# Kernel optimization log

Measured on AMD Instinct MI355X. Metric: run time of the kernel, lower is better.

Reference implementation:

```python
import jax, jax.numpy as jnp
import numpy as np

N = 6144          # nodes
F_IN = 512        # num_feature
HID = 64          # hidden_dim
C = 40            # num_class
H = 3             # num_heads
ALPHA = 0.2       # leaky relu slope
NEG_INF = -9e15


def gat_layer(x, adj, W, a_src, a_dst):
    # x: [N, f_in], W: [H, f_in, f_out], a_src/a_dst: [H, f_out]
    Wh = jnp.einsum('nf,hfo->hno', x, W)                  # [H, N, f_out]
    e_src = jnp.einsum('hno,ho->hn', Wh, a_src)           # [H, N]
    e_dst = jnp.einsum('hno,ho->hn', Wh, a_dst)           # [H, N]
    e = jax.nn.leaky_relu(e_src[:, :, None] + e_dst[:, None, :], ALPHA)  # [H, N, N]
    scores = jnp.where(adj > 0, e, NEG_INF)               # mask non-edges
    attn = jax.nn.softmax(scores, axis=-1)                # softmax over neighbors
    out = jnp.einsum('hnm,hmo->hno', attn, Wh)            # [H, N, f_out]
    return out.mean(axis=0)                               # average heads -> [N, f_out]


def setup_inputs() -> dict:
    key = jax.random.key(0)
    k = jax.random.split(key, 8)
    feature = jax.random.normal(k[0], (N, F_IN), dtype=jnp.float32)
    adj = (jax.random.uniform(k[1], (N, N)) < 0.01).astype(jnp.float32)
    adj = jnp.maximum(adj, jnp.eye(N, dtype=jnp.float32))
    s1 = 1.0 / np.sqrt(F_IN)
    s2 = 1.0 / np.sqrt(HID)
    W1 = jax.random.normal(k[2], (H, F_IN, HID), dtype=jnp.float32) * s1
    a1_src = jax.random.normal(k[3], (H, HID), dtype=jnp.float32) * s2
    a1_dst = jax.random.normal(k[4], (H, HID), dtype=jnp.float32) * s2
    W2 = jax.random.normal(k[5], (H, HID, C), dtype=jnp.float32) * s2
    a2_src = jax.random.normal(k[6], (H, C), dtype=jnp.float32) * (1.0 / np.sqrt(C))
    a2_dst = jax.random.normal(k[7], (H, C), dtype=jnp.float32) * (1.0 / np.sqrt(C))
    return {"feature": feature, "adj": adj, "W1": W1, "a1_src": a1_src,
            "a1_dst": a1_dst, "W2": W2, "a2_src": a2_src, "a2_dst": a2_dst}


def reference(feature, adj, W1, a1_src, a1_dst, W2, a2_src, a2_dst):
    # eval mode: dropout is identity
    x = jax.nn.relu(gat_layer(feature, adj, W1, a1_src, a1_dst))  # [N, HID]
    x = gat_layer(x, adj, W2, a2_src, a2_dst)                     # [N, C]
    return jax.nn.log_softmax(x, axis=1)
```

## Files before the change

### kernel.cpp

```cpp
#include <hip/hip_runtime.h>
#include <math.h>

#define NN   6144
#define FIN  512
#define HIDN 64
#define NC   40
#define NH   3
#define CAP  128
#define NCHUNK (CAP / 64)
#define LALPHA 0.2f
#define KSPLIT 4
#define PK_LOW  0x3FFFu
#define PK_HIGH 0xFFFFC000u

typedef unsigned long long ull;

__device__ __forceinline__ float bf2f(ushort s) {
    return __uint_as_float((unsigned)s << 16);
}
__device__ __forceinline__ ushort f2bf(float f) {
    unsigned u = __float_as_uint(f);
    return (ushort)((u + 0x7FFFu + ((u >> 16) & 1u)) >> 16);
}

__global__ __launch_bounds__(256) void k_csr(const float* __restrict__ adj,
                                             int* __restrict__ nbr,
                                             int* __restrict__ deg) {
    __shared__ int lidx[4][64];
    __shared__ int wtot[4];
    int row  = blockIdx.x;
    int wid  = threadIdx.x >> 6;
    int lane = threadIdx.x & 63;
    const float* base = adj + (size_t)row * NN + wid * (NN / 4);
    ull below = (1ull << lane) - 1ull;
    int cnt = 0;
#pragma unroll
    for (int ch = 0; ch < 6; ch++) {
        float4 v = *reinterpret_cast<const float4*>(base + ch * 256 + lane * 4);
        bool h0 = v.x > 0.f, h1 = v.y > 0.f, h2 = v.z > 0.f, h3 = v.w > 0.f;
        ull b0 = __ballot(h0), b1 = __ballot(h1), b2 = __ballot(h2), b3 = __ballot(h3);
        int p = cnt + __popcll(b0 & below) + __popcll(b1 & below)
                    + __popcll(b2 & below) + __popcll(b3 & below);
        int col = wid * (NN / 4) + ch * 256 + lane * 4;
        if (h0) { if (p < 64) lidx[wid][p] = col + 0; p++; }
        if (h1) { if (p < 64) lidx[wid][p] = col + 1; p++; }
        if (h2) { if (p < 64) lidx[wid][p] = col + 2; p++; }
        if (h3) { if (p < 64) lidx[wid][p] = col + 3; p++; }
        cnt += __popcll(b0) + __popcll(b1) + __popcll(b2) + __popcll(b3);
    }
    if (lane == 0) wtot[wid] = cnt;
    __syncthreads();
    int t0 = wtot[0], t1 = wtot[1], t2 = wtot[2], t3 = wtot[3];
    int wb = (wid > 0 ? t0 : 0) + (wid > 1 ? t1 : 0) + (wid > 2 ? t2 : 0);
    int total = t0 + t1 + t2 + t3;
    if (threadIdx.x == 0) deg[row] = total < CAP ? total : CAP;
    int myc = wtot[wid] < 64 ? wtot[wid] : 64;
    if (lane < myc) {
        int pos = wb + lane;
        if (pos < CAP) nbr[(size_t)row * CAP + pos] = lidx[wid][lane];
    }
}

__global__ __launch_bounds__(256) void k_gemm1(const float* __restrict__ x,
                                               const float* __restrict__ W,
                                               float* __restrict__ Whp) {
    __shared__ float xs[64][68];
    __shared__ float wsh[64][68];
    int h  = blockIdx.y;
    int n0 = blockIdx.x * 64;
    int kz = blockIdx.z;
    int tid = threadIdx.x;
    int og4 = (tid & 15) * 4;
    int mg4 = (tid >> 4) * 4;

    float acc[4][4] = {{0.f}};
    const float* xbase0 = x + (size_t)n0 * FIN;
    const float* wbase0 = W + (size_t)h * FIN * HIDN;

    for (int t = 0; t < 2; t++) {
        int k0 = kz * 128 + t * 64;
#pragma unroll
        for (int i = 0; i < 4; i++) {
            int l = tid + i * 256;
            int r = l >> 4;
            int c = (l & 15) * 4;
            *reinterpret_cast<float4*>(&xs[r][c]) =
                *reinterpret_cast<const float4*>(xbase0 + (size_t)r * FIN + k0 + c);
            *reinterpret_cast<float4*>(&wsh[r][c]) =
                *reinterpret_cast<const float4*>(wbase0 + (size_t)(k0 + r) * HIDN + c);
        }
        __syncthreads();

#pragma unroll 8
        for (int k = 0; k < 64; k += 4) {
            float4 xv[4], wv[4];
            xv[0] = *reinterpret_cast<const float4*>(&xs[mg4 + 0][k]);
            xv[1] = *reinterpret_cast<const float4*>(&xs[mg4 + 1][k]);
            xv[2] = *reinterpret_cast<const float4*>(&xs[mg4 + 2][k]);
            xv[3] = *reinterpret_cast<const float4*>(&xs[mg4 + 3][k]);
            wv[0] = *reinterpret_cast<const float4*>(&wsh[k + 0][og4]);
            wv[1] = *reinterpret_cast<const float4*>(&wsh[k + 1][og4]);
            wv[2] = *reinterpret_cast<const float4*>(&wsh[k + 2][og4]);
            wv[3] = *reinterpret_cast<const float4*>(&wsh[k + 3][og4]);
            const float* xf = reinterpret_cast<const float*>(xv);
            const float* wf = reinterpret_cast<const float*>(wv);
#pragma unroll
            for (int i = 0; i < 4; i++) {
#pragma unroll
                for (int kk = 0; kk < 4; kk++) {
                    float xval = xf[i * 4 + kk];
#pragma unroll
                    for (int j = 0; j < 4; j++)
                        acc[i][j] += xval * wf[kk * 4 + j];
                }
            }
        }
        __syncthreads();
    }

    float* outp = Whp + (((size_t)kz * NH + h) * NN + n0 + mg4) * HIDN + og4;
#pragma unroll
    for (int i = 0; i < 4; i++) {
        float4 v = make_float4(acc[i][0], acc[i][1], acc[i][2], acc[i][3]);
        *reinterpret_cast<float4*>(outp + (size_t)i * HIDN) = v;
    }
}

__global__ __launch_bounds__(256) void k_sum_e1(const float* __restrict__ Whp,
                                                const float* __restrict__ a_src,
                                                const float* __restrict__ a_dst,
                                                ushort* __restrict__ Whb,
                                                float* __restrict__ es,
                                                float* __restrict__ ed) {
    int gw   = blockIdx.x * 4 + (threadIdx.x >> 6);
    int lane = threadIdx.x & 63;
    int h = gw / NN, n = gw % NN;
    size_t idx = ((size_t)h * NN + n) * HIDN + lane;
    size_t stride = (size_t)NH * NN * HIDN;
    float v = Whp[idx] + Whp[idx + stride] + Whp[idx + 2 * stride] + Whp[idx + 3 * stride];
    Whb[idx] = f2bf(v);
    float s = v * a_src[h * HIDN + lane];
    float d = v * a_dst[h * HIDN + lane];
#pragma unroll
    for (int off = 32; off; off >>= 1) {
        s += __shfl_xor(s, off);
        d += __shfl_xor(d, off);
    }
    if (lane == 0) { es[h * NN + n] = s; ed[h * NN + n] = d; }
}

__global__ __launch_bounds__(192) void k_attn1f(const int* __restrict__ nbr,
                                                const int* __restrict__ deg,
                                                const ushort* __restrict__ Whb,
                                                const float* __restrict__ es,
                                                const float* __restrict__ ed,
                                                const float* __restrict__ W2,
                                                const float* __restrict__ a2s,
                                                const float* __restrict__ a2d,
                                                ushort* __restrict__ Wh2b,
                                                float* __restrict__ e2s,
                                                float* __restrict__ e2d) {
    __shared__ unsigned pks[NH][CAP];
    __shared__ float hsum[NH][HIDN];
    int n = blockIdx.x;
    int h = threadIdx.x >> 6;
    int lane = threadIdx.x & 63;
    int d = deg[n];
    const int* nrow = nbr + (size_t)n * CAP;
    float esv = es[h * NN + n];

    float psum = 0.f;
#pragma unroll
    for (int c = 0; c < NCHUNK; c++) {
        int k = c * 64 + lane;
        unsigned u = 0;
        if (k < d) {
            int mm = nrow[k];
            float e = esv + ed[h * NN + mm];
            float s = e > 0.f ? e : LALPHA * e;
            float p = __expf(s);
            u = (__float_as_uint(p) & PK_HIGH) | (unsigned)mm;
            psum += __uint_as_float(u & PK_HIGH);
        }
        pks[h][k] = u;
    }
#pragma unroll
    for (int off = 32; off; off >>= 1) psum += __shfl_xor(psum, off);
    float inv = 1.f / psum;
    __syncthreads();

    const ushort* WhH = Whb + (size_t)h * NN * HIDN + lane;
    float a0 = 0.f, a1 = 0.f, a2 = 0.f, a3 = 0.f;
    int iters = (d + 3) >> 2;
    for (int g = 0; g < iters; g++) {
        uint4 uu = *reinterpret_cast<const uint4*>(&pks[h][g * 4]);
        a0 += __uint_as_float(uu.x & PK_HIGH) * bf2f(WhH[(size_t)(uu.x & PK_LOW) * HIDN]);
        a1 += __uint_as_float(uu.y & PK_HIGH) * bf2f(WhH[(size_t)(uu.y & PK_LOW) * HIDN]);
        a2 += __uint_as_float(uu.z & PK_HIGH) * bf2f(WhH[(size_t)(uu.z & PK_LOW) * HIDN]);
        a3 += __uint_as_float(uu.w & PK_HIGH) * bf2f(WhH[(size_t)(uu.w & PK_LOW) * HIDN]);
    }
    float hacc = ((a0 + a1) + (a2 + a3));
    hsum[h][lane] = hacc * inv;
    __syncthreads();

    float xv = (hsum[0][lane] + hsum[1][lane] + hsum[2][lane]) * (1.f / NH);
    xv = fmaxf(xv, 0.f);

    int c = lane < NC ? lane : NC - 1;
    float acc = 0.f;
#pragma unroll 8
    for (int o = 0; o < HIDN; o++) {
        float xb = __shfl(xv, o);
        float wv = W2[((size_t)h * HIDN + o) * NC + c];
        acc += xb * wv;
    }
    if (lane >= NC) acc = 0.f;

    float s2 = acc * (lane < NC ? a2s[h * NC + lane] : 0.f);
    float d2 = acc * (lane < NC ? a2d[h * NC + lane] : 0.f);
#pragma unroll
    for (int off = 32; off; off >>= 1) {
        s2 += __shfl_xor(s2, off);
        d2 += __shfl_xor(d2, off);
    }
    if (lane < NC) Wh2b[((size_t)h * NN + n) * NC + lane] = f2bf(acc);
    if (lane == 0) { e2s[h * NN + n] = s2; e2d[h * NN + n] = d2; }
}

__global__ __launch_bounds__(192) void k_attn2(const int* __restrict__ nbr,
                                               const int* __restrict__ deg,
                                               const ushort* __restrict__ Wh2b,
                                               const float* __restrict__ es,
                                               const float* __restrict__ ed,
                                               float* __restrict__ out) {
    __shared__ unsigned pks[NH][CAP];
    __shared__ float hsum[NH][HIDN];
    int n = blockIdx.x;
    int h = threadIdx.x >> 6;
    int lane = threadIdx.x & 63;
    int d = deg[n];
    const int* nrow = nbr + (size_t)n * CAP;
    float esv = es[h * NN + n];

    float psum = 0.f;
#pragma unroll
    for (int c = 0; c < NCHUNK; c++) {
        int k = c * 64 + lane;
        unsigned u = 0;
        if (k < d) {
            int mm = nrow[k];
            float e = esv + ed[h * NN + mm];
            float s = e > 0.f ? e : LALPHA * e;
            float p = __expf(s);
            u = (__float_as_uint(p) & PK_HIGH) | (unsigned)mm;
            psum += __uint_as_float(u & PK_HIGH);
        }
        pks[h][k] = u;
    }
#pragma unroll
    for (int off = 32; off; off >>= 1) psum += __shfl_xor(psum, off);
    float inv = 1.f / psum;
    __syncthreads();

    const ushort* W2H = Wh2b + (size_t)h * NN * NC + (lane < NC ? lane : 0);
    float a0 = 0.f, a1 = 0.f, a2 = 0.f, a3 = 0.f;
    int iters = (d + 3) >> 2;
    for (int g = 0; g < iters; g++) {
        uint4 uu = *reinterpret_cast<const uint4*>(&pks[h][g * 4]);
        a0 += __uint_as_float(uu.x & PK_HIGH) * bf2f(W2H[(size_t)(uu.x & PK_LOW) * NC]);
        a1 += __uint_as_float(uu.y & PK_HIGH) * bf2f(W2H[(size_t)(uu.y & PK_LOW) * NC]);
        a2 += __uint_as_float(uu.z & PK_HIGH) * bf2f(W2H[(size_t)(uu.z & PK_LOW) * NC]);
        a3 += __uint_as_float(uu.w & PK_HIGH) * bf2f(W2H[(size_t)(uu.w & PK_LOW) * NC]);
    }
    float hacc = ((a0 + a1) + (a2 + a3));
    if (lane < NC) hsum[h][lane] = hacc * inv;
    __syncthreads();

    if (threadIdx.x < 64) {
        float a = (lane < NC)
            ? (hsum[0][lane] + hsum[1][lane] + hsum[2][lane]) * (1.f / NH)
            : -INFINITY;
        float mx = a;
#pragma unroll
        for (int off = 32; off; off >>= 1) mx = fmaxf(mx, __shfl_xor(mx, off));
        float ex = (lane < NC) ? __expf(a - mx) : 0.f;
        float se = ex;
#pragma unroll
        for (int off = 32; off; off >>= 1) se += __shfl_xor(se, off);
        if (lane < NC) out[(size_t)n * NC + lane] = a - mx - logf(se);
    }
}

extern "C" void kernel_launch(void* const* d_in, const int* in_sizes, int n_in,
                              void* d_out, int out_size, void* d_ws, size_t ws_size,
                              hipStream_t stream) {
    const float* feature = (const float*)d_in[0];
    const float* adj     = (const float*)d_in[1];
    const float* W1      = (const float*)d_in[2];
    const float* a1_src  = (const float*)d_in[3];
    const float* a1_dst  = (const float*)d_in[4];
    const float* W2      = (const float*)d_in[5];
    const float* a2_src  = (const float*)d_in[6];
    const float* a2_dst  = (const float*)d_in[7];
    float* out = (float*)d_out;

    char* ws = (char*)d_ws;
    size_t off = 0;
    int*    nbr = (int*)(ws + off);    off += (size_t)NN * CAP * sizeof(int);
    int*    deg = (int*)(ws + off);    off += (size_t)NN * sizeof(int);
    float*  Whp = (float*)(ws + off);  off += (size_t)KSPLIT * NH * NN * HIDN * sizeof(float);
    ushort* Whb = (ushort*)(ws + off); off += (size_t)NH * NN * HIDN * sizeof(ushort);
    float*  e1s = (float*)(ws + off);  off += (size_t)NH * NN * sizeof(float);
    float*  e1d = (float*)(ws + off);  off += (size_t)NH * NN * sizeof(float);
    ushort* Wh2b= (ushort*)(ws + off); off += (size_t)NH * NN * NC * sizeof(ushort);
    float*  e2s = (float*)(ws + off);  off += (size_t)NH * NN * sizeof(float);
    float*  e2d = (float*)(ws + off);  off += (size_t)NH * NN * sizeof(float);

    k_csr<<<NN, 256, 0, stream>>>(adj, nbr, deg);
    k_gemm1<<<dim3(NN / 64, NH, KSPLIT), 256, 0, stream>>>(feature, W1, Whp);
    k_sum_e1<<<(NH * NN) / 4, 256, 0, stream>>>(Whp, a1_src, a1_dst, Whb, e1s, e1d);
    k_attn1f<<<NN, 192, 0, stream>>>(nbr, deg, Whb, e1s, e1d, W2, a2_src, a2_dst,
                                     Wh2b, e2s, e2d);
    k_attn2<<<NN, 192, 0, stream>>>(nbr, deg, Wh2b, e2s, e2d, out);
}
```

Baseline: 102.0 us.

## Fuse adjacency-to-CSR compaction into the first attention kernel

Removes the separate k_csr kernel and performs the ballot-based adjacency row compaction inside k_attn1f, where each of the three head wavefronts scans a third of the row. The neighbor list is kept in shared memory for layer-1 attention and also written to global memory for layer 2. This drops one kernel launch and the round trip of reading the neighbor list back from global memory. In exchange, the 150MB adjacency scan now runs with 192 threads per block inside the attention kernel, which could lengthen that kernel and add LDS pressure.

Result: faster. 96.73 us (-5.2%).

```diff
diff --git a/kernel.cpp b/kernel.cpp
--- a/kernel.cpp
+++ b/kernel.cpp
@@ -21,44 +21,6 @@
 __device__ __forceinline__ ushort f2bf(float f) {
     unsigned u = __float_as_uint(f);
     return (ushort)((u + 0x7FFFu + ((u >> 16) & 1u)) >> 16);
-}
-
-__global__ __launch_bounds__(256) void k_csr(const float* __restrict__ adj,
-                                             int* __restrict__ nbr,
-                                             int* __restrict__ deg) {
-    __shared__ int lidx[4][64];
-    __shared__ int wtot[4];
-    int row  = blockIdx.x;
-    int wid  = threadIdx.x >> 6;
-    int lane = threadIdx.x & 63;
-    const float* base = adj + (size_t)row * NN + wid * (NN / 4);
-    ull below = (1ull << lane) - 1ull;
-    int cnt = 0;
-#pragma unroll
-    for (int ch = 0; ch < 6; ch++) {
-        float4 v = *reinterpret_cast<const float4*>(base + ch * 256 + lane * 4);
-        bool h0 = v.x > 0.f, h1 = v.y > 0.f, h2 = v.z > 0.f, h3 = v.w > 0.f;
-        ull b0 = __ballot(h0), b1 = __ballot(h1), b2 = __ballot(h2), b3 = __ballot(h3);
-        int p = cnt + __popcll(b0 & below) + __popcll(b1 & below)
-                    + __popcll(b2 & below) + __popcll(b3 & below);
-        int col = wid * (NN / 4) + ch * 256 + lane * 4;
-        if (h0) { if (p < 64) lidx[wid][p] = col + 0; p++; }
-        if (h1) { if (p < 64) lidx[wid][p] = col + 1; p++; }
-        if (h2) { if (p < 64) lidx[wid][p] = col + 2; p++; }
-        if (h3) { if (p < 64) lidx[wid][p] = col + 3; p++; }
-        cnt += __popcll(b0) + __popcll(b1) + __popcll(b2) + __popcll(b3);
-    }
-    if (lane == 0) wtot[wid] = cnt;
-    __syncthreads();
-    int t0 = wtot[0], t1 = wtot[1], t2 = wtot[2], t3 = wtot[3];
-    int wb = (wid > 0 ? t0 : 0) + (wid > 1 ? t1 : 0) + (wid > 2 ? t2 : 0);
-    int total = t0 + t1 + t2 + t3;
-    if (threadIdx.x == 0) deg[row] = total < CAP ? total : CAP;
-    int myc = wtot[wid] < 64 ? wtot[wid] : 64;
-    if (lane < myc) {
-        int pos = wb + lane;
-        if (pos < CAP) nbr[(size_t)row * CAP + pos] = lidx[wid][lane];
-    }
 }
 
 __global__ __launch_bounds__(256) void k_gemm1(const float* __restrict__ x,
@@ -149,8 +111,9 @@
     if (lane == 0) { es[h * NN + n] = s; ed[h * NN + n] = d; }
 }
 
-__global__ __launch_bounds__(192) void k_attn1f(const int* __restrict__ nbr,
-                                                const int* __restrict__ deg,
+__global__ __launch_bounds__(192) void k_attn1f(const float* __restrict__ adj,
+                                                int* __restrict__ nbr,
+                                                int* __restrict__ deg,
                                                 const ushort* __restrict__ Whb,
                                                 const float* __restrict__ es,
                                                 const float* __restrict__ ed,
@@ -160,22 +123,58 @@
                                                 ushort* __restrict__ Wh2b,
                                                 float* __restrict__ e2s,
                                                 float* __restrict__ e2d) {
+    __shared__ int stage[NH][64];
+    __shared__ int wtot[NH];
+    __shared__ int nbrL[CAP];
     __shared__ unsigned pks[NH][CAP];
     __shared__ float hsum[NH][HIDN];
+
     int n = blockIdx.x;
     int h = threadIdx.x >> 6;
     int lane = threadIdx.x & 63;
-    int d = deg[n];
-    const int* nrow = nbr + (size_t)n * CAP;
+
+    {
+        const float* base = adj + (size_t)n * NN + h * 2048;
+        ull below = (1ull << lane) - 1ull;
+        int cnt = 0;
+#pragma unroll
+        for (int ch = 0; ch < 8; ch++) {
+            float4 v = *reinterpret_cast<const float4*>(base + ch * 256 + lane * 4);
+            bool h0 = v.x > 0.f, h1 = v.y > 0.f, h2 = v.z > 0.f, h3 = v.w > 0.f;
+            ull b0 = __ballot(h0), b1 = __ballot(h1), b2 = __ballot(h2), b3 = __ballot(h3);
+            int p = cnt + __popcll(b0 & below) + __popcll(b1 & below)
+                        + __popcll(b2 & below) + __popcll(b3 & below);
+            int col = h * 2048 + ch * 256 + lane * 4;
+            if (h0) { if (p < 64) stage[h][p] = col + 0; p++; }
+            if (h1) { if (p < 64) stage[h][p] = col + 1; p++; }
+            if (h2) { if (p < 64) stage[h][p] = col + 2; p++; }
+            if (h3) { if (p < 64) stage[h][p] = col + 3; p++; }
+            cnt += __popcll(b0) + __popcll(b1) + __popcll(b2) + __popcll(b3);
+        }
+        if (lane == 0) wtot[h] = cnt;
+    }
+    __syncthreads();
+    int t0 = wtot[0], t1 = wtot[1], t2 = wtot[2];
+    int pre = (h > 0 ? t0 : 0) + (h > 1 ? t1 : 0);
+    int d = t0 + t1 + t2;
+    if (d > CAP) d = CAP;
+    {
+        int myc = wtot[h] < 64 ? wtot[h] : 64;
+        if (lane < myc && pre + lane < CAP) nbrL[pre + lane] = stage[h][lane];
+    }
+    __syncthreads();
+    if (threadIdx.x < CAP) nbr[(size_t)n * CAP + threadIdx.x] =
+        ((int)threadIdx.x < d) ? nbrL[threadIdx.x] : 0;
+    if (threadIdx.x == 0) deg[n] = d;
+
     float esv = es[h * NN + n];
-
     float psum = 0.f;
 #pragma unroll
     for (int c = 0; c < NCHUNK; c++) {
         int k = c * 64 + lane;
         unsigned u = 0;
         if (k < d) {
-            int mm = nrow[k];
+            int mm = nbrL[k];
             float e = esv + ed[h * NN + mm];
             float s = e > 0.f ? e : LALPHA * e;
             float p = __expf(s);
@@ -316,10 +315,9 @@
     float*  e2s = (float*)(ws + off);  off += (size_t)NH * NN * sizeof(float);
     float*  e2d = (float*)(ws + off);  off += (size_t)NH * NN * sizeof(float);
 
-    k_csr<<<NN, 256, 0, stream>>>(adj, nbr, deg);
     k_gemm1<<<dim3(NN / 64, NH, KSPLIT), 256, 0, stream>>>(feature, W1, Whp);
     k_sum_e1<<<(NH * NN) / 4, 256, 0, stream>>>(Whp, a1_src, a1_dst, Whb, e1s, e1d);
-    k_attn1f<<<NN, 192, 0, stream>>>(nbr, deg, Whb, e1s, e1d, W2, a2_src, a2_dst,
+    k_attn1f<<<NN, 192, 0, stream>>>(adj, nbr, deg, Whb, e1s, e1d, W2, a2_src, a2_dst,
                                      Wh2b, e2s, e2d);
     k_attn2<<<NN, 192, 0, stream>>>(nbr, deg, Wh2b, e2s, e2d, out);
 }
```
